# Kernel optimization log

Hardware: AMD Instinct MI355X
Metric: run time of the kernel (lower is better)

## Reference

```python
import jax, jax.numpy as jnp
import numpy as np

# ----- config (mirrors SpatialAxis init) -----
B, N = 1, 32768
D_MODEL, NHEAD, DEPTH = 256, 8, 2
COORD = 3
PATCH = 512          # self.patch_size default
BITS = 10            # self.morton_bits default
SHIFT = True         # self.shift_order default
MLP_H = 4 * D_MODEL
HD = D_MODEL // NHEAD
EPS = 1e-5


def _part1by2(v):
    # spread low 10 bits of int32 so there are 2 zero bits between each
    v = v & 0x000003FF
    v = (v | (v << 16)) & 0x030000FF
    v = (v | (v << 8)) & 0x0300F00F
    v = (v | (v << 4)) & 0x030C30C3
    v = (v | (v << 2)) & 0x09249249
    return v


def _perm_for_block(coords, i):
    # Z-order (Morton) serialization with per-block axis rotation; odd blocks
    # shift the order by half a patch (shifted-window style). Returns [B,N] int32.
    c = jax.lax.stop_gradient(coords)[..., np.roll(np.arange(COORD), -i)]
    cmin = c.min(axis=1, keepdims=True)
    cmax = c.max(axis=1, keepdims=True)
    q = ((c - cmin) / (cmax - cmin + 1e-9) * (2 ** BITS - 1)).astype(jnp.int32)
    q = jnp.clip(q, 0, 2 ** BITS - 1)
    code = (_part1by2(q[..., 0]) | (_part1by2(q[..., 1]) << 1)
            | (_part1by2(q[..., 2]) << 2))  # [B,N]
    perm = jnp.argsort(code, axis=1)
    if SHIFT and (i % 2 == 1):
        perm = jnp.roll(perm, PATCH // 2, axis=1)
    return perm


def _ln(x, g, b):
    m = x.mean(-1, keepdims=True)
    v = x.var(-1, keepdims=True)
    return (x - m) * jax.lax.rsqrt(v + EPS) * g + b


def _point_block(xs, cs, p):
    # xs: [M, P, D] tokens of one patch each; cs: [M, P, 3]
    M, P, D = xs.shape
    h = _ln(xs, p['ln1_g'], p['ln1_b'])
    qkv = h @ p['w_qkv'] + p['b_qkv']                         # [M,P,3D]
    q, k, v = jnp.split(qkv, 3, axis=-1)
    q = q.reshape(M, P, NHEAD, HD)
    k = k.reshape(M, P, NHEAD, HD)
    v = v.reshape(M, P, NHEAD, HD)
    scores = jnp.einsum('mphd,mqhd->mhpq', q, k) / np.sqrt(HD).astype(np.float32)
    rel = cs[:, :, None, :] - cs[:, None, :, :]               # [M,P,P,3]
    bias = jnp.einsum('mpqc,ch->mhpq', rel, p['w_pos']) + p['b_pos'][None, :, None, None]
    attn = jax.nn.softmax(scores + bias, axis=-1)
    o = jnp.einsum('mhpq,mqhd->mphd', attn, v).reshape(M, P, D)
    xs = xs + o @ p['w_proj'] + p['b_proj']
    h2 = _ln(xs, p['ln2_g'], p['ln2_b'])
    xs = xs + jax.nn.gelu(h2 @ p['w_fc1'] + p['b_fc1']) @ p['w_fc2'] + p['b_fc2']
    return xs


def _forward(x, coords, params):
    Cc = coords.shape[-1]
    nblk = N // PATCH
    for i in range(DEPTH):
        p = {k: v[i] for k, v in params.items()}
        perm = _perm_for_block(coords, i)                      # [B,N]
        inv = jnp.argsort(perm, axis=1)
        x_s = jnp.take_along_axis(x, perm[:, :, None], axis=1)
        c_s = jnp.take_along_axis(coords, perm[:, :, None], axis=1)
        x_f = x_s.reshape(B * nblk, PATCH, D_MODEL)
        c_f = c_s.reshape(B * nblk, PATCH, Cc)
        y = _point_block(x_f, c_f, p).reshape(B, N, D_MODEL)
        x = jnp.take_along_axis(y, inv[:, :, None], axis=1)
    return _ln(x, params['norm_g'][0], params['norm_b'][0])


def setup_inputs() -> dict:
    key = jax.random.key(0)
    ks = jax.random.split(key, 20)
    s = 0.02
    d = {
        'x': jax.random.normal(ks[0], (B, N, D_MODEL), jnp.float32),
        'coords': jax.random.uniform(ks[1], (B, N, COORD), jnp.float32),
        'ln1_g': jnp.ones((DEPTH, D_MODEL), jnp.float32),
        'ln1_b': jnp.zeros((DEPTH, D_MODEL), jnp.float32),
        'w_qkv': jax.random.normal(ks[2], (DEPTH, D_MODEL, 3 * D_MODEL), jnp.float32) * s,
        'b_qkv': jnp.zeros((DEPTH, 3 * D_MODEL), jnp.float32),
        'w_proj': jax.random.normal(ks[3], (DEPTH, D_MODEL, D_MODEL), jnp.float32) * s,
        'b_proj': jnp.zeros((DEPTH, D_MODEL), jnp.float32),
        'w_pos': jax.random.normal(ks[4], (DEPTH, COORD, NHEAD), jnp.float32) * s,
        'b_pos': jnp.zeros((DEPTH, NHEAD), jnp.float32),
        'ln2_g': jnp.ones((DEPTH, D_MODEL), jnp.float32),
        'ln2_b': jnp.zeros((DEPTH, D_MODEL), jnp.float32),
        'w_fc1': jax.random.normal(ks[5], (DEPTH, D_MODEL, MLP_H), jnp.float32) * s,
        'b_fc1': jnp.zeros((DEPTH, MLP_H), jnp.float32),
        'w_fc2': jax.random.normal(ks[6], (DEPTH, MLP_H, D_MODEL), jnp.float32) * s,
        'b_fc2': jnp.zeros((DEPTH, D_MODEL), jnp.float32),
        'norm_g': jnp.ones((1, D_MODEL), jnp.float32),
        'norm_b': jnp.zeros((1, D_MODEL), jnp.float32),
    }
    return d


def reference(x, coords, ln1_g, ln1_b, w_qkv, b_qkv, w_proj, b_proj, w_pos, b_pos,
              ln2_g, ln2_b, w_fc1, b_fc1, w_fc2, b_fc2, norm_g, norm_b):
    params = dict(ln1_g=ln1_g, ln1_b=ln1_b, w_qkv=w_qkv, b_qkv=b_qkv,
                  w_proj=w_proj, b_proj=b_proj, w_pos=w_pos, b_pos=b_pos,
                  ln2_g=ln2_g, ln2_b=ln2_b, w_fc1=w_fc1, b_fc1=b_fc1,
                  w_fc2=w_fc2, b_fc2=b_fc2, norm_g=norm_g, norm_b=norm_b)
    return _forward(x, coords, params)
```

## Files before the change

### kernel.cpp

```cpp
#include <hip/hip_runtime.h>

typedef unsigned long long u64;
typedef unsigned int u32;
typedef unsigned short u16;
typedef float f32x4 __attribute__((ext_vector_type(4)));
typedef __bf16 bf16x8 __attribute__((ext_vector_type(8)));

#define N_TOK 32768

__device__ inline u16 f2bf(float f){
  u32 x = __float_as_uint(f);
  u32 r = x + 0x7FFFu + ((x >> 16) & 1u);
  return (u16)(r >> 16);
}

__device__ inline u16 f2bf_hw(float f){
  u32 pk;
  asm("v_cvt_pk_bf16_f32 %0, %1, %2" : "=v"(pk) : "v"(f), "v"(0.f));
  return (u16)pk;
}

__device__ inline f32x4 mfma16(bf16x8 a, bf16x8 b, f32x4 c){
  return __builtin_amdgcn_mfma_f32_16x16x32_bf16(a, b, c, 0, 0, 0);
}

__device__ inline float fexp2(float x){
  float r;
  asm("v_exp_f32 %0, %1" : "=v"(r) : "v"(x));
  return r;
}
__device__ inline float frcp(float x){
  float r;
  asm("v_rcp_f32 %0, %1" : "=v"(r) : "v"(x));
  return r;
}

typedef const __attribute__((address_space(1))) unsigned int* gas_ptr;
typedef __attribute__((address_space(3))) unsigned int* las_ptr;
__device__ inline void gload_lds16(const u16* g, u16* l){
  __builtin_amdgcn_global_load_lds((gas_ptr)g, (las_ptr)l, 16, 0, 0);
}

__device__ inline u32 rp_idx(const u64* __restrict__ keys, int j, int shift){
  return (u32)(keys[(j + N_TOK - shift) & (N_TOK - 1)] & 0xFFFFull);
}

__device__ inline float gelu_tanh(float x){
  float u = 0.7978845608028654f * (x + 0.044715f * x * x * x);
  float e = fexp2(2.8853900817779268f * u);
  return 0.5f * x * (2.0f - 2.0f * frcp(e + 1.0f));
}

__device__ inline u32 part1by2(u32 v){
  v &= 0x3FFu;
  v = (v | (v << 16)) & 0x030000FFu;
  v = (v | (v << 8))  & 0x0300F00Fu;
  v = (v | (v << 4))  & 0x030C30C3u;
  v = (v | (v << 2))  & 0x09249249u;
  return v;
}

__device__ inline void ce64(u64& a, u64& b, bool asc){
  u64 lo = a < b ? a : b;
  u64 hi = a < b ? b : a;
  a = asc ? lo : hi;
  b = asc ? hi : lo;
}

__device__ inline int xcd_swz(int bid, int nwg){
  int cpx = nwg >> 3;
  return (bid & 7) * cpx + (bid >> 3);
}

__global__ void minmax_init(u32* __restrict__ cmm){
  int t = threadIdx.x;
  if (t < 3) cmm[t] = 0xFFFFFFFFu;
  else if (t < 6) cmm[t] = 0u;
}

__global__ void __launch_bounds__(256) minmax_atomic(const float* __restrict__ coords,
                                                     u32* __restrict__ cmm){
  __shared__ u32 smn[3], smx[3];
  int t = threadIdx.x;
  if (t < 3){ smn[t] = 0xFFFFFFFFu; smx[t] = 0u; }
  __syncthreads();
  int i = blockIdx.x * 256 + t;
  u32 bits = __float_as_uint(coords[i]);
  int a = i % 3;
  atomicMin(&smn[a], bits);
  atomicMax(&smx[a], bits);
  __syncthreads();
  if (t < 3){
    atomicMin(&cmm[t], smn[t]);
    atomicMax(&cmm[3 + t], smx[t]);
  }
}

__global__ void __launch_bounds__(256) wprep_all(
    const float* __restrict__ w_qkv, const float* __restrict__ w_proj,
    const float* __restrict__ w_fc1, const float* __restrict__ w_fc2,
    u16* __restrict__ d_qkv, u16* __restrict__ d_proj,
    u16* __restrict__ d_fc1, u16* __restrict__ d_fc2){
  int b = blockIdx.x;
  const float* src; u16* dst; int K, Nn;
  if (b < 384){ src = w_qkv; dst = d_qkv; K = 256; Nn = 768; }
  else if (b < 512){ b -= 384; src = w_proj; dst = d_proj; K = 256; Nn = 256; }
  else if (b < 1024){ b -= 512; src = w_fc1; dst = d_fc1; K = 256; Nn = 1024; }
  else { b -= 1024; src = w_fc2; dst = d_fc2; K = 1024; Nn = 256; }
  int ntx = Nn >> 5;
  int tpl = (K >> 5) * ntx;
  int layer = b / tpl, tb = b % tpl;
  src += (size_t)layer * K * Nn;
  dst += (size_t)layer * K * Nn;
  int tk = tb / ntx, tn = tb % ntx;
  __shared__ float tile[32][33];
  int r = threadIdx.x >> 5, c = threadIdx.x & 31;
  for (int rr = r; rr < 32; rr += 8)
    tile[rr][c] = src[(size_t)(tk*32 + rr) * Nn + tn*32 + c];
  __syncthreads();
  for (int rr = r; rr < 32; rr += 8)
    dst[(size_t)(tn*32 + rr) * K + tk*32 + c] = f2bf(tile[c][rr]);
}

__global__ void __launch_bounds__(256) codes_kernel(const float* __restrict__ coords,
                                                    const float* __restrict__ cmm,
                                                    u64* __restrict__ keys){
  int p = blockIdx.x * 256 + threadIdx.x;
  int layer = p >> 15, t = p & (N_TOK - 1);
  u32 code = 0;
  #pragma unroll
  for (int j = 0; j < 3; ++j){
    int ax = (j + layer) % 3;
    float c = coords[t*3 + ax];
    float mn = cmm[ax], mx = cmm[3 + ax];
    float v = (c - mn) / (mx - mn + 1e-9f) * 1023.0f;
    int q = (int)v;
    q = q < 0 ? 0 : (q > 1023 ? 1023 : q);
    code |= part1by2((u32)q) << j;
  }
  keys[p] = ((u64)code << 16) | (u32)t;
}

__global__ void __launch_bounds__(64) sort_wave1024(u64* __restrict__ keys){
  int chunk = blockIdx.x;
  int lane = threadIdx.x;
  int base = chunk * 1024 + lane * 16;
  int bl = base & (N_TOK - 1);
  u64 v[16];
  #pragma unroll
  for (int p = 0; p < 16; ++p) v[p] = keys[base + p];
  #pragma unroll
  for (int k2 = 2; k2 <= 16; k2 <<= 1){
    #pragma unroll
    for (int j = k2 >> 1; j > 0; j >>= 1){
      #pragma unroll
      for (int p = 0; p < 16; ++p){
        if ((p & j) == 0){
          bool asc = (((bl + p) & k2) == 0);
          ce64(v[p], v[p+j], asc);
        }
      }
    }
  }
  #pragma unroll
  for (int kk = 32; kk <= 1024; kk <<= 1){
    bool asc = ((bl & kk) == 0);
    #pragma unroll
    for (int j = kk >> 1; j >= 16; j >>= 1){
      int m = j >> 4;
      bool kmin = asc != ((lane & m) != 0);
      #pragma unroll
      for (int p = 0; p < 16; ++p){
        u64 pv = __shfl_xor(v[p], m);
        u64 mn = v[p] < pv ? v[p] : pv;
        u64 mx = v[p] < pv ? pv : v[p];
        v[p] = kmin ? mn : mx;
      }
    }
    #pragma unroll
    for (int j = 8; j > 0; j >>= 1)
      #pragma unroll
      for (int p = 0; p < 16; ++p)
        if ((p & j) == 0) ce64(v[p], v[p+j], asc);
  }
  #pragma unroll
  for (int p = 0; p < 16; ++p) keys[base + p] = v[p];
}

template<int R>
__global__ void __launch_bounds__(256) sort_strided(u64* __restrict__ keys, int logJ, int k){
  const int E = 1 << R;
  int gps = N_TOK >> R;
  int tid = blockIdx.x * 256 + threadIdx.x;
  int seg = tid / gps, gamma = tid % gps;
  int high = gamma >> logJ, low = gamma & ((1 << logJ) - 1);
  int base = seg * N_TOK + (high << (logJ + R)) + low;
  u64 v[E];
  #pragma unroll
  for (int m = 0; m < E; ++m) v[m] = keys[base + (m << logJ)];
  bool asc = (((base & (N_TOK - 1)) & k) == 0);
  #pragma unroll
  for (int jj = R - 1; jj >= 0; --jj)
    #pragma unroll
    for (int m = 0; m < E; ++m)
      if ((m & (1 << jj)) == 0) ce64(v[m], v[m + (1 << jj)], asc);
  #pragma unroll
  for (int m = 0; m < E; ++m) keys[base + (m << logJ)] = v[m];
}

__global__ void __launch_bounds__(64) sort_tail1024(u64* __restrict__ keys, int k){
  int chunk = blockIdx.x;
  int lane = threadIdx.x;
  int base = chunk * 1024 + lane * 16;
  bool asc = ((((chunk * 1024) & (N_TOK - 1)) & k) == 0);
  u64 v[16];
  #pragma unroll
  for (int p = 0; p < 16; ++p) v[p] = keys[base + p];
  #pragma unroll
  for (int m = 32; m >= 1; m >>= 1){
    bool kmin = asc != ((lane & m) != 0);
    #pragma unroll
    for (int p = 0; p < 16; ++p){
      u64 pv = __shfl_xor(v[p], m);
      u64 mn = v[p] < pv ? v[p] : pv;
      u64 mx = v[p] < pv ? pv : v[p];
      v[p] = kmin ? mn : mx;
    }
  }
  #pragma unroll
  for (int j = 8; j > 0; j >>= 1)
    #pragma unroll
    for (int p = 0; p < 16; ++p)
      if ((p & j) == 0) ce64(v[p], v[p+j], asc);
  #pragma unroll
  for (int p = 0; p < 16; ++p) keys[base + p] = v[p];
}

__global__ void __launch_bounds__(256) gather_ln1_kernel(
    const float* __restrict__ xin, const float* __restrict__ coords,
    const u64* __restrict__ keys, int shift,
    const float* __restrict__ g1, const float* __restrict__ b1,
    const float* __restrict__ wpos,
    float* __restrict__ dproj, u16* __restrict__ h){
  int w = threadIdx.x >> 6, lane = threadIdx.x & 63;
  int j = blockIdx.x * 4 + w;
  u32 src = rp_idx(keys, j, shift);
  float4 v = ((const float4*)xin)[(size_t)src * 64 + lane];
  float s = v.x + v.y + v.z + v.w;
  for (int m = 1; m < 64; m <<= 1) s += __shfl_xor(s, m);
  float mean = s * (1.0f / 256.0f);
  float dx = v.x - mean, dy = v.y - mean, dz = v.z - mean, dw = v.w - mean;
  float q = dx*dx + dy*dy + dz*dz + dw*dw;
  for (int m = 1; m < 64; m <<= 1) q += __shfl_xor(q, m);
  float rs = rsqrtf(q * (1.0f / 256.0f) + 1e-5f);
  int c0 = lane * 4;
  u16 h0 = f2bf(dx * rs * g1[c0+0] + b1[c0+0]);
  u16 h1 = f2bf(dy * rs * g1[c0+1] + b1[c0+1]);
  u16 h2 = f2bf(dz * rs * g1[c0+2] + b1[c0+2]);
  u16 h3 = f2bf(dw * rs * g1[c0+3] + b1[c0+3]);
  uint2 pk; pk.x = (u32)h0 | ((u32)h1 << 16); pk.y = (u32)h2 | ((u32)h3 << 16);
  *(uint2*)&h[(size_t)j * 256 + c0] = pk;
  if (lane < 8){
    float acc = 0.0f;
    #pragma unroll
    for (int c = 0; c < 3; ++c) acc += coords[(size_t)src*3 + c] * wpos[c*8 + lane];
    dproj[(size_t)j * 8 + lane] = acc;
  }
}

__global__ void __launch_bounds__(256) ln_bf16_kernel(const float* __restrict__ xin,
    const float* __restrict__ g, const float* __restrict__ b, u16* __restrict__ out){
  int w = threadIdx.x >> 6, lane = threadIdx.x & 63;
  int j = blockIdx.x * 4 + w;
  float4 v = ((const float4*)xin)[(size_t)j * 64 + lane];
  float s = v.x + v.y + v.z + v.w;
  for (int m = 1; m < 64; m <<= 1) s += __shfl_xor(s, m);
  float mean = s * (1.0f / 256.0f);
  float dx = v.x - mean, dy = v.y - mean, dz = v.z - mean, dw = v.w - mean;
  float q = dx*dx + dy*dy + dz*dz + dw*dw;
  for (int m = 1; m < 64; m <<= 1) q += __shfl_xor(q, m);
  float rs = rsqrtf(q * (1.0f / 256.0f) + 1e-5f);
  int c0 = lane * 4;
  u16 h0 = f2bf(dx * rs * g[c0+0] + b[c0+0]);
  u16 h1 = f2bf(dy * rs * g[c0+1] + b[c0+1]);
  u16 h2 = f2bf(dz * rs * g[c0+2] + b[c0+2]);
  u16 h3 = f2bf(dw * rs * g[c0+3] + b[c0+3]);
  uint2 pk; pk.x = (u32)h0 | ((u32)h1 << 16); pk.y = (u32)h2 | ((u32)h3 << 16);
  *(uint2*)&out[(size_t)j * 256 + c0] = pk;
}

__global__ void __launch_bounds__(256) ln_final_kernel(const float* __restrict__ xin,
    const float* __restrict__ g, const float* __restrict__ b, float* __restrict__ out){
  int w = threadIdx.x >> 6, lane = threadIdx.x & 63;
  int j = blockIdx.x * 4 + w;
  float4 v = ((const float4*)xin)[(size_t)j * 64 + lane];
  float s = v.x + v.y + v.z + v.w;
  for (int m = 1; m < 64; m <<= 1) s += __shfl_xor(s, m);
  float mean = s * (1.0f / 256.0f);
  float dx = v.x - mean, dy = v.y - mean, dz = v.z - mean, dw = v.w - mean;
  float q = dx*dx + dy*dy + dz*dz + dw*dw;
  for (int m = 1; m < 64; m <<= 1) q += __shfl_xor(q, m);
  float rs = rsqrtf(q * (1.0f / 256.0f) + 1e-5f);
  int c0 = lane * 4;
  float4 o;
  o.x = dx * rs * g[c0+0] + b[c0+0];
  o.y = dy * rs * g[c0+1] + b[c0+1];
  o.z = dz * rs * g[c0+2] + b[c0+2];
  o.w = dw * rs * g[c0+3] + b[c0+3];
  ((float4*)out)[(size_t)j * 64 + lane] = o;
}

template<int EPI, int BN>
__global__ void __launch_bounds__(1024) gemm2_kernel(
    const u16* __restrict__ A, const u16* __restrict__ Wt,
    const float* __restrict__ bias, int K, int Nn,
    u16* __restrict__ outb, float* __restrict__ outf,
    const float* __restrict__ res, const u64* __restrict__ keys, int shift){
  constexpr int WN = (BN == 256) ? 4 : 2;
  constexpr int WM = 16 / WN;
  constexpr int MI = (256 / WM) / 16;
  constexpr int NI = (BN / WN) / 16;
  constexpr int SPANM = 256 / WM;
  constexpr int SPANN = BN / WN;
  __shared__ __align__(16) u16 As[2][256 * 32];
  __shared__ __align__(16) u16 Bs[2][BN * 32];
  int swz = xcd_swz(blockIdx.x, gridDim.x);
  int ntiles = Nn / BN;
  int m0 = (swz / ntiles) * 256;
  int n0 = (swz % ntiles) * BN;
  int tid = threadIdx.x;
  int lane = tid & 63, lc = lane & 15, g = lane >> 4;
  int w = tid >> 6;
  int wm = (BN == 256) ? (w >> 2) : (w >> 1);
  int wn = (BN == 256) ? (w & 3) : (w & 1);
  f32x4 acc[MI][NI];
  #pragma unroll
  for (int mi = 0; mi < MI; ++mi)
    #pragma unroll
    for (int ni = 0; ni < NI; ++ni) acc[mi][ni] = (f32x4){0.f,0.f,0.f,0.f};
  int rA = tid >> 2, sA = tid & 3;
  const u16* Ag = A + (size_t)(m0 + rA) * K + (sA ^ ((rA >> 1) & 3)) * 8;
  int cb = (BN == 256) ? tid : (tid & 511);
  int rB = cb >> 2, sB = cb & 3;
  const u16* Bg = Wt + (size_t)(n0 + rB) * K + (sB ^ ((rB >> 1) & 3)) * 8;
  int aofs = (tid & ~63) * 8;
  int bofs = (cb & ~63) * 8;
  int nt = K >> 5;
  auto issue = [&](int t, int b){
    int kk = t << 5;
    gload_lds16(Ag + kk, As[b] + aofs);
    gload_lds16(Bg + kk, Bs[b] + bofs);
  };
  issue(0, 0);
  int cur = 0;
  int fsw = (lc >> 1) & 3;
  for (int t = 0; t < nt; ++t){
    if (t + 1 < nt){
      issue(t + 1, cur ^ 1);
      asm volatile("s_waitcnt vmcnt(2)" ::: "memory");
    } else {
      asm volatile("s_waitcnt vmcnt(0)" ::: "memory");
    }
    __builtin_amdgcn_s_barrier();
    bf16x8 af[MI], bfr[NI];
    #pragma unroll
    for (int mi = 0; mi < MI; ++mi)
      af[mi] = *(const bf16x8*)&As[cur][(wm*SPANM + mi*16 + lc)*32 + (g ^ fsw)*8];
    #pragma unroll
    for (int ni = 0; ni < NI; ++ni)
      bfr[ni] = *(const bf16x8*)&Bs[cur][(wn*SPANN + ni*16 + lc)*32 + (g ^ fsw)*8];
    #pragma unroll
    for (int mi = 0; mi < MI; ++mi)
      #pragma unroll
      for (int ni = 0; ni < NI; ++ni)
        acc[mi][ni] = mfma16(af[mi], bfr[ni], acc[mi][ni]);
    asm volatile("" ::: "memory");
    __builtin_amdgcn_s_barrier();
    cur ^= 1;
  }
  #pragma unroll
  for (int ni = 0; ni < NI; ++ni){
    int col = n0 + wn*SPANN + ni*16 + lc;
    float bv = bias[col];
    #pragma unroll
    for (int mi = 0; mi < MI; ++mi){
      #pragma unroll
      for (int r = 0; r < 4; ++r){
        int row = m0 + wm*SPANM + mi*16 + g*4 + r;
        float v = acc[mi][ni][r] + bv;
        if constexpr (EPI == 0){
          if (col < 256) v *= 0.25500526f;
          outb[(size_t)row * Nn + col] = f2bf_hw(v);
        } else if constexpr (EPI == 1){
          outb[(size_t)row * Nn + col] = f2bf_hw(gelu_tanh(v));
        } else {
          u32 dst = rp_idx(keys, row, shift);
          outf[(size_t)dst * 256 + col] = res[(size_t)row * 256 + col] + v;
        }
      }
    }
  }
}

template<int EPI>
__global__ void __launch_bounds__(256) gemm_kernel(
    const u16* __restrict__ A, const u16* __restrict__ Wt,
    const float* __restrict__ bias, int K, int Nn,
    u16* __restrict__ outb, float* __restrict__ outf,
    const float* __restrict__ res, const u64* __restrict__ keys, int shift){
  __shared__ __align__(16) u16 As[2][128 * 32];
  __shared__ __align__(16) u16 Bs[2][128 * 32];
  int swz = xcd_swz(blockIdx.x, gridDim.x);
  int ntiles = Nn / 128;
  int m0 = (swz / ntiles) * 128;
  int n0 = (swz % ntiles) * 128;
  int tid = threadIdx.x;
  int lane = tid & 63, lc = lane & 15, g = lane >> 4;
  int w = tid >> 6, wm = w >> 1, wn = w & 1;
  f32x4 acc[4][4];
  #pragma unroll
  for (int mi = 0; mi < 4; ++mi)
    #pragma unroll
    for (int ni = 0; ni < 4; ++ni) acc[mi][ni] = (f32x4){0.f,0.f,0.f,0.f};
  int r1 = tid >> 2, s1 = tid & 3;
  int r2 = r1 + 64;
  int sw = s1 ^ ((r1 >> 1) & 3);
  const u16* Ag1 = A  + (size_t)(m0 + r1) * K + sw*8;
  const u16* Ag2 = A  + (size_t)(m0 + r2) * K + sw*8;
  const u16* Bg1 = Wt + (size_t)(n0 + r1) * K + sw*8;
  const u16* Bg2 = Wt + (size_t)(n0 + r2) * K + sw*8;
  int wofs = (tid & ~63) * 8;
  int nt = K >> 5;
  gload_lds16(Ag1, As[0] + wofs);
  gload_lds16(Ag2, As[0] + wofs + 2048);
  gload_lds16(Bg1, Bs[0] + wofs);
  gload_lds16(Bg2, Bs[0] + wofs + 2048);
  int cur = 0;
  int fsw = (lc >> 1) & 3;
  for (int t = 0; t < nt; ++t){
    if (t + 1 < nt){
      int kk = (t + 1) << 5;
      gload_lds16(Ag1 + kk, As[cur^1] + wofs);
      gload_lds16(Ag2 + kk, As[cur^1] + wofs + 2048);
      gload_lds16(Bg1 + kk, Bs[cur^1] + wofs);
      gload_lds16(Bg2 + kk, Bs[cur^1] + wofs + 2048);
      asm volatile("s_waitcnt vmcnt(4)" ::: "memory");
    } else {
      asm volatile("s_waitcnt vmcnt(0)" ::: "memory");
    }
    __builtin_amdgcn_s_barrier();
    bf16x8 af[4], bfr[4];
    #pragma unroll
    for (int mi = 0; mi < 4; ++mi)
      af[mi] = *(const bf16x8*)&As[cur][(wm*64 + mi*16 + lc)*32 + (g ^ fsw)*8];
    #pragma unroll
    for (int ni = 0; ni < 4; ++ni)
      bfr[ni] = *(const bf16x8*)&Bs[cur][(wn*64 + ni*16 + lc)*32 + (g ^ fsw)*8];
    #pragma unroll
    for (int mi = 0; mi < 4; ++mi)
      #pragma unroll
      for (int ni = 0; ni < 4; ++ni)
        acc[mi][ni] = mfma16(af[mi], bfr[ni], acc[mi][ni]);
    asm volatile("" ::: "memory");
    __builtin_amdgcn_s_barrier();
    cur ^= 1;
  }
  #pragma unroll
  for (int ni = 0; ni < 4; ++ni){
    int col = n0 + wn*64 + ni*16 + lc;
    float bv = bias[col];
    #pragma unroll
    for (int mi = 0; mi < 4; ++mi){
      #pragma unroll
      for (int r = 0; r < 4; ++r){
        int row = m0 + wm*64 + mi*16 + g*4 + r;
        float v = acc[mi][ni][r] + bv;
        if constexpr (EPI == 2){
          u32 src = rp_idx(keys, row, shift);
          outf[(size_t)row * 256 + col] = res[(size_t)src * 256 + col] + v;
        } else {
          outb[(size_t)row * Nn + col] = f2bf_hw(v);
        }
      }
    }
  }
}

#define VSTR 516
#define ATTN_LDS (512*32*2 + 32*VSTR*2 + 512*2)
__global__ void __launch_bounds__(512) attn_kernel(
    const u16* __restrict__ qkvb, const float* __restrict__ dproj,
    u16* __restrict__ o){
  extern __shared__ char smem[];
  u16* Kl = (u16*)smem;
  u16* Vt = (u16*)(smem + 512*32*2);
  u16* wl = (u16*)(smem + 512*32*2 + 32*VSTR*2);
  int h = blockIdx.x & 7;
  int base = (blockIdx.x >> 3) * 512;
  int tid = threadIdx.x, w = tid >> 6, lane = tid & 63, lc = lane & 15, g = lane >> 4;
  const float L2E = 1.4426950408889634f;
  for (int i = tid; i < 2048; i += 512){
    int j = i >> 2, s = i & 3;
    int swc = s ^ ((j >> 1) & 3);
    *(uint4*)&Kl[j*32 + s*8] =
      *(const uint4*)&qkvb[(size_t)(base + j)*768 + 256 + h*32 + swc*8];
  }
  for (int i = tid; i < 1024; i += 512){
    int p = i >> 2, d0 = (i & 3) * 8;
    int j0 = 2*p, j1 = j0 + 1;
    float wv0 = fexp2(-L2E * dproj[(size_t)(base + j0)*8 + h]);
    float wv1 = fexp2(-L2E * dproj[(size_t)(base + j1)*8 + h]);
    uint4 r0 = *(const uint4*)&qkvb[(size_t)(base + j0)*768 + 512 + h*32 + d0];
    uint4 r1 = *(const uint4*)&qkvb[(size_t)(base + j1)*768 + 512 + h*32 + d0];
    const u16* p0 = (const u16*)&r0; const u16* p1 = (const u16*)&r1;
    int j5 = j0 & 31, b = j5 >> 4, m = j5 & 15;
    int slot = (j0 & ~31) + 8*(m >> 2) + 4*b + (m & 3);
    #pragma unroll
    for (int e = 0; e < 8; ++e){
      float f0 = __uint_as_float(((u32)p0[e]) << 16) * wv0;
      float f1 = __uint_as_float(((u32)p1[e]) << 16) * wv1;
      u32 pk;
      asm("v_cvt_pk_bf16_f32 %0, %1, %2" : "=v"(pk) : "v"(f0), "v"(f1));
      *(u32*)&Vt[(d0 + e)*VSTR + slot] = pk;
    }
    if (d0 == 0){
      u32 pkw;
      asm("v_cvt_pk_bf16_f32 %0, %1, %2" : "=v"(pkw) : "v"(wv0), "v"(wv1));
      *(u32*)&wl[slot] = pkw;
    }
  }
  __syncthreads();
  const f32x4 zf = {0.f,0.f,0.f,0.f};
  const u16* Qg = qkvb + (size_t)base*768 + h*32;
  int fswk = (lc >> 1) & 3;
  for (int t = 0; t < 4; ++t){
    int q0 = w*64 + t*16;
    bf16x8 qf = *(const bf16x8*)&Qg[(size_t)(q0 + lc)*768 + g*8];
    f32x4 oa0 = zf, oa1 = zf, la = zf;
    f32x4 ob0 = zf, ob1 = zf, lb = zf;
    #pragma unroll 4
    for (int grp = 0; grp < 16; ++grp){
      int kb = grp * 32;
      bf16x8 kf0 = *(const bf16x8*)&Kl[(kb + lc)*32 + (g ^ fswk)*8];
      bf16x8 kf1 = *(const bf16x8*)&Kl[(kb + 16 + lc)*32 + (g ^ fswk)*8];
      f32x4 s0 = mfma16(kf0, qf, zf);
      f32x4 s1 = mfma16(kf1, qf, zf);
      #pragma unroll
      for (int r = 0; r < 4; ++r){
        s0[r] = fexp2(s0[r]);
        s1[r] = fexp2(s1[r]);
      }
      u32 pk0, pk1, pk2, pk3;
      asm("v_cvt_pk_bf16_f32 %0, %1, %2" : "=v"(pk0) : "v"(s0[0]), "v"(s0[1]));
      asm("v_cvt_pk_bf16_f32 %0, %1, %2" : "=v"(pk1) : "v"(s0[2]), "v"(s0[3]));
      asm("v_cvt_pk_bf16_f32 %0, %1, %2" : "=v"(pk2) : "v"(s1[0]), "v"(s1[1]));
      asm("v_cvt_pk_bf16_f32 %0, %1, %2" : "=v"(pk3) : "v"(s1[2]), "v"(s1[3]));
      bf16x8 pf;
      ((u32*)&pf)[0] = pk0; ((u32*)&pf)[1] = pk1;
      ((u32*)&pf)[2] = pk2; ((u32*)&pf)[3] = pk3;
      bf16x8 v0, v1;
      *(uint2*)&v0       = *(const uint2*)&Vt[lc*VSTR + kb + g*8];
      *((uint2*)&v0 + 1) = *(const uint2*)&Vt[lc*VSTR + kb + g*8 + 4];
      *(uint2*)&v1       = *(const uint2*)&Vt[(16+lc)*VSTR + kb + g*8];
      *((uint2*)&v1 + 1) = *(const uint2*)&Vt[(16+lc)*VSTR + kb + g*8 + 4];
      bf16x8 wf = *(const bf16x8*)&wl[kb + g*8];
      __builtin_amdgcn_s_setprio(1);
      if (grp & 1){
        ob0 = mfma16(pf, v0, ob0);
        ob1 = mfma16(pf, v1, ob1);
        lb  = mfma16(pf, wf, lb);
      } else {
        oa0 = mfma16(pf, v0, oa0);
        oa1 = mfma16(pf, v1, oa1);
        la  = mfma16(pf, wf, la);
      }
      __builtin_amdgcn_s_setprio(0);
    }
    #pragma unroll
    for (int r = 0; r < 4; ++r){
      float inv = frcp(la[r] + lb[r]);
      size_t tok = (size_t)(base + q0 + g*4 + r);
      o[tok*256 + h*32 + lc]      = f2bf((oa0[r] + ob0[r]) * inv);
      o[tok*256 + h*32 + 16 + lc] = f2bf((oa1[r] + ob1[r]) * inv);
    }
  }
}

extern "C" void kernel_launch(void* const* d_in, const int* in_sizes, int n_in,
                              void* d_out, int out_size, void* d_ws, size_t ws_size,
                              hipStream_t stream){
  const float* x      = (const float*)d_in[0];
  const float* coords = (const float*)d_in[1];
  const float* ln1_g  = (const float*)d_in[2];
  const float* ln1_b  = (const float*)d_in[3];
  const float* w_qkv  = (const float*)d_in[4];
  const float* b_qkv  = (const float*)d_in[5];
  const float* w_proj = (const float*)d_in[6];
  const float* b_proj = (const float*)d_in[7];
  const float* w_pos  = (const float*)d_in[8];
  const float* ln2_g  = (const float*)d_in[10];
  const float* ln2_b  = (const float*)d_in[11];
  const float* w_fc1  = (const float*)d_in[12];
  const float* b_fc1  = (const float*)d_in[13];
  const float* w_fc2  = (const float*)d_in[14];
  const float* b_fc2  = (const float*)d_in[15];
  const float* norm_g = (const float*)d_in[16];
  const float* norm_b = (const float*)d_in[17];
  float* outp = (float*)d_out;

  hipFuncSetAttribute((const void*)attn_kernel,
                      hipFuncAttributeMaxDynamicSharedMemorySize, ATTN_LDS);

  char* ws = (char*)d_ws;
  size_t off = 0;
  auto alloc = [&](size_t bytes) -> void* {
    void* p = ws + off;
    off += (bytes + 255) & ~(size_t)255;
    return p;
  };
  u64*   keys   = (u64*)  alloc((size_t)2 * N_TOK * 8);
  float* cmm    = (float*)alloc(256);
  float* dproj  = (float*)alloc((size_t)N_TOK * 8 * 4);
  u16*   h      = (u16*)  alloc((size_t)N_TOK * 256 * 2);
  u16*   qkvb   = (u16*)  alloc((size_t)N_TOK * 768 * 2);
  float* x2     = (float*)alloc((size_t)N_TOK * 256 * 4);
  u16*   t      = (u16*)  alloc((size_t)N_TOK * 1024 * 2);
  float* xA     = (float*)alloc((size_t)N_TOK * 256 * 4);
  u16*   wtqkv  = (u16*)  alloc((size_t)2 * 256 * 768 * 2);
  u16*   wtproj = (u16*)  alloc((size_t)2 * 256 * 256 * 2);
  u16*   wtfc1  = (u16*)  alloc((size_t)2 * 256 * 1024 * 2);
  u16*   wtfc2  = (u16*)  alloc((size_t)2 * 1024 * 256 * 2);
  u16*   o      = t;
  float* xB     = (float*)qkvb;
  (void)in_sizes; (void)n_in; (void)out_size; (void)ws_size;

  minmax_init<<<1, 64, 0, stream>>>((u32*)cmm);
  minmax_atomic<<<384, 256, 0, stream>>>(coords, (u32*)cmm);
  wprep_all<<<1536, 256, 0, stream>>>(w_qkv, w_proj, w_fc1, w_fc2,
                                      wtqkv, wtproj, wtfc1, wtfc2);

  codes_kernel<<<256, 256, 0, stream>>>(coords, cmm, keys);
  sort_wave1024<<<64, 64, 0, stream>>>(keys);
  sort_strided<1><<<128, 256, 0, stream>>>(keys, 10, 2048);
  sort_tail1024<<<64, 64, 0, stream>>>(keys, 2048);
  sort_strided<2><<<64, 256, 0, stream>>>(keys, 10, 4096);
  sort_tail1024<<<64, 64, 0, stream>>>(keys, 4096);
  sort_strided<3><<<32, 256, 0, stream>>>(keys, 10, 8192);
  sort_tail1024<<<64, 64, 0, stream>>>(keys, 8192);
  sort_strided<3><<<32, 256, 0, stream>>>(keys, 11, 16384);
  sort_strided<1><<<128, 256, 0, stream>>>(keys, 10, 16384);
  sort_tail1024<<<64, 64, 0, stream>>>(keys, 16384);
  sort_strided<3><<<32, 256, 0, stream>>>(keys, 12, 32768);
  sort_strided<2><<<64, 256, 0, stream>>>(keys, 10, 32768);
  sort_tail1024<<<64, 64, 0, stream>>>(keys, 32768);

  for (int layer = 0; layer < 2; ++layer){
    int shift = (layer & 1) ? 256 : 0;
    const float* xin = (layer == 0) ? x : xA;
    float* xout = (layer == 0) ? xA : xB;
    u64* keyL = keys + (size_t)layer * N_TOK;

    gather_ln1_kernel<<<8192, 256, 0, stream>>>(xin, coords, keyL, shift,
        ln1_g + layer*256, ln1_b + layer*256, w_pos + layer*24, dproj, h);
    gemm2_kernel<0,256><<<384, 1024, 0, stream>>>(h, wtqkv + (size_t)layer*768*256,
        b_qkv + layer*768, 256, 768, qkvb, nullptr, nullptr, nullptr, 0);
    attn_kernel<<<512, 512, ATTN_LDS, stream>>>(qkvb, dproj, o);
    gemm_kernel<2><<<512, 256, 0, stream>>>(o, wtproj + (size_t)layer*256*256,
        b_proj + layer*256, 256, 256, nullptr, x2, xin, keyL, shift);
    ln_bf16_kernel<<<8192, 256, 0, stream>>>(x2, ln2_g + layer*256, ln2_b + layer*256, h);
    gemm2_kernel<1,256><<<512, 1024, 0, stream>>>(h, wtfc1 + (size_t)layer*1024*256,
        b_fc1 + layer*1024, 256, 1024, t, nullptr, nullptr, nullptr, 0);
    gemm2_kernel<3,128><<<256, 1024, 0, stream>>>(t, wtfc2 + (size_t)layer*256*1024,
        b_fc2 + layer*256, 1024, 256, nullptr, xout, x2, keyL, shift);
  }
  ln_final_kernel<<<8192, 256, 0, stream>>>(xB, norm_g, norm_b, outp);
}
```

Baseline: 473.6 us.

## Fuse proj GEMM with residual and LayerNorm2; process two query tiles per attention iteration

```diff
diff --git a/kernel.cpp b/kernel.cpp
--- a/kernel.cpp
+++ b/kernel.cpp
@@ -268,27 +268,6 @@
   }
 }
 
-__global__ void __launch_bounds__(256) ln_bf16_kernel(const float* __restrict__ xin,
-    const float* __restrict__ g, const float* __restrict__ b, u16* __restrict__ out){
-  int w = threadIdx.x >> 6, lane = threadIdx.x & 63;
-  int j = blockIdx.x * 4 + w;
-  float4 v = ((const float4*)xin)[(size_t)j * 64 + lane];
-  float s = v.x + v.y + v.z + v.w;
-  for (int m = 1; m < 64; m <<= 1) s += __shfl_xor(s, m);
-  float mean = s * (1.0f / 256.0f);
-  float dx = v.x - mean, dy = v.y - mean, dz = v.z - mean, dw = v.w - mean;
-  float q = dx*dx + dy*dy + dz*dz + dw*dw;
-  for (int m = 1; m < 64; m <<= 1) q += __shfl_xor(q, m);
-  float rs = rsqrtf(q * (1.0f / 256.0f) + 1e-5f);
-  int c0 = lane * 4;
-  u16 h0 = f2bf(dx * rs * g[c0+0] + b[c0+0]);
-  u16 h1 = f2bf(dy * rs * g[c0+1] + b[c0+1]);
-  u16 h2 = f2bf(dz * rs * g[c0+2] + b[c0+2]);
-  u16 h3 = f2bf(dw * rs * g[c0+3] + b[c0+3]);
-  uint2 pk; pk.x = (u32)h0 | ((u32)h1 << 16); pk.y = (u32)h2 | ((u32)h3 << 16);
-  *(uint2*)&out[(size_t)j * 256 + c0] = pk;
-}
-
 __global__ void __launch_bounds__(256) ln_final_kernel(const float* __restrict__ xin,
     const float* __restrict__ g, const float* __restrict__ b, float* __restrict__ out){
   int w = threadIdx.x >> 6, lane = threadIdx.x & 63;
@@ -402,49 +381,43 @@
   }
 }
 
-template<int EPI>
-__global__ void __launch_bounds__(256) gemm_kernel(
+__global__ void __launch_bounds__(1024) gemm2ln_kernel(
     const u16* __restrict__ A, const u16* __restrict__ Wt,
-    const float* __restrict__ bias, int K, int Nn,
-    u16* __restrict__ outb, float* __restrict__ outf,
-    const float* __restrict__ res, const u64* __restrict__ keys, int shift){
-  __shared__ __align__(16) u16 As[2][128 * 32];
-  __shared__ __align__(16) u16 Bs[2][128 * 32];
+    const float* __restrict__ bias,
+    const u64* __restrict__ keys, int shift, const float* __restrict__ res,
+    const float* __restrict__ g2, const float* __restrict__ b2,
+    float* __restrict__ x2out, u16* __restrict__ hout){
+  __shared__ __align__(16) u16 As[2][256 * 32];
+  __shared__ __align__(16) u16 Bs[2][256 * 32];
+  __shared__ float red_s[256][4];
+  __shared__ float red_q[256][4];
+  const int K = 256;
   int swz = xcd_swz(blockIdx.x, gridDim.x);
-  int ntiles = Nn / 128;
-  int m0 = (swz / ntiles) * 128;
-  int n0 = (swz % ntiles) * 128;
+  int m0 = swz * 256;
   int tid = threadIdx.x;
   int lane = tid & 63, lc = lane & 15, g = lane >> 4;
-  int w = tid >> 6, wm = w >> 1, wn = w & 1;
+  int w = tid >> 6, wm = w >> 2, wn = w & 3;
   f32x4 acc[4][4];
   #pragma unroll
   for (int mi = 0; mi < 4; ++mi)
     #pragma unroll
     for (int ni = 0; ni < 4; ++ni) acc[mi][ni] = (f32x4){0.f,0.f,0.f,0.f};
-  int r1 = tid >> 2, s1 = tid & 3;
-  int r2 = r1 + 64;
-  int sw = s1 ^ ((r1 >> 1) & 3);
-  const u16* Ag1 = A  + (size_t)(m0 + r1) * K + sw*8;
-  const u16* Ag2 = A  + (size_t)(m0 + r2) * K + sw*8;
-  const u16* Bg1 = Wt + (size_t)(n0 + r1) * K + sw*8;
-  const u16* Bg2 = Wt + (size_t)(n0 + r2) * K + sw*8;
-  int wofs = (tid & ~63) * 8;
-  int nt = K >> 5;
-  gload_lds16(Ag1, As[0] + wofs);
-  gload_lds16(Ag2, As[0] + wofs + 2048);
-  gload_lds16(Bg1, Bs[0] + wofs);
-  gload_lds16(Bg2, Bs[0] + wofs + 2048);
+  int rA = tid >> 2, sA = tid & 3;
+  const u16* Ag = A  + (size_t)(m0 + rA) * K + (sA ^ ((rA >> 1) & 3)) * 8;
+  const u16* Bg = Wt + (size_t)rA * K + (sA ^ ((rA >> 1) & 3)) * 8;
+  int aofs = (tid & ~63) * 8;
+  auto issue = [&](int t, int b){
+    int kk = t << 5;
+    gload_lds16(Ag + kk, As[b] + aofs);
+    gload_lds16(Bg + kk, Bs[b] + aofs);
+  };
+  issue(0, 0);
   int cur = 0;
   int fsw = (lc >> 1) & 3;
-  for (int t = 0; t < nt; ++t){
-    if (t + 1 < nt){
-      int kk = (t + 1) << 5;
-      gload_lds16(Ag1 + kk, As[cur^1] + wofs);
-      gload_lds16(Ag2 + kk, As[cur^1] + wofs + 2048);
-      gload_lds16(Bg1 + kk, Bs[cur^1] + wofs);
-      gload_lds16(Bg2 + kk, Bs[cur^1] + wofs + 2048);
-      asm volatile("s_waitcnt vmcnt(4)" ::: "memory");
+  for (int t = 0; t < 8; ++t){
+    if (t + 1 < 8){
+      issue(t + 1, cur ^ 1);
+      asm volatile("s_waitcnt vmcnt(2)" ::: "memory");
     } else {
       asm volatile("s_waitcnt vmcnt(0)" ::: "memory");
     }
@@ -465,22 +438,53 @@
     __builtin_amdgcn_s_barrier();
     cur ^= 1;
   }
+  float bv[4], g2v[4], b2v[4];
   #pragma unroll
   for (int ni = 0; ni < 4; ++ni){
-    int col = n0 + wn*64 + ni*16 + lc;
-    float bv = bias[col];
-    #pragma unroll
-    for (int mi = 0; mi < 4; ++mi){
-      #pragma unroll
-      for (int r = 0; r < 4; ++r){
-        int row = m0 + wm*64 + mi*16 + g*4 + r;
-        float v = acc[mi][ni][r] + bv;
-        if constexpr (EPI == 2){
-          u32 src = rp_idx(keys, row, shift);
-          outf[(size_t)row * 256 + col] = res[(size_t)src * 256 + col] + v;
-        } else {
-          outb[(size_t)row * Nn + col] = f2bf_hw(v);
-        }
+    int col = wn*64 + ni*16 + lc;
+    bv[ni] = bias[col];
+    g2v[ni] = g2[col];
+    b2v[ni] = b2[col];
+  }
+  #pragma unroll
+  for (int mi = 0; mi < 4; ++mi){
+    #pragma unroll
+    for (int r = 0; r < 4; ++r){
+      int lrow = wm*64 + mi*16 + g*4 + r;
+      int grow = m0 + lrow;
+      u32 src = rp_idx(keys, grow, shift);
+      float sp = 0.f, qp = 0.f;
+      #pragma unroll
+      for (int ni = 0; ni < 4; ++ni){
+        int col = wn*64 + ni*16 + lc;
+        float v = acc[mi][ni][r] + bv[ni] + res[(size_t)src*256 + col];
+        sp += v; qp += v*v;
+        x2out[(size_t)grow*256 + col] = v;
+      }
+      sp += __shfl_xor(sp, 1); sp += __shfl_xor(sp, 2);
+      sp += __shfl_xor(sp, 4); sp += __shfl_xor(sp, 8);
+      qp += __shfl_xor(qp, 1); qp += __shfl_xor(qp, 2);
+      qp += __shfl_xor(qp, 4); qp += __shfl_xor(qp, 8);
+      if (lc == 0){ red_s[lrow][wn] = sp; red_q[lrow][wn] = qp; }
+    }
+  }
+  __syncthreads();
+  #pragma unroll
+  for (int mi = 0; mi < 4; ++mi){
+    #pragma unroll
+    for (int r = 0; r < 4; ++r){
+      int lrow = wm*64 + mi*16 + g*4 + r;
+      int grow = m0 + lrow;
+      float s = red_s[lrow][0] + red_s[lrow][1] + red_s[lrow][2] + red_s[lrow][3];
+      float q = red_q[lrow][0] + red_q[lrow][1] + red_q[lrow][2] + red_q[lrow][3];
+      float mean = s * (1.0f / 256.0f);
+      float var = q * (1.0f / 256.0f) - mean * mean;
+      float rs = rsqrtf(var + 1e-5f);
+      #pragma unroll
+      for (int ni = 0; ni < 4; ++ni){
+        int col = wn*64 + ni*16 + lc;
+        float v = x2out[(size_t)grow*256 + col];
+        hout[(size_t)grow*256 + col] = f2bf_hw((v - mean) * rs * g2v[ni] + b2v[ni]);
       }
     }
   }
@@ -533,9 +537,10 @@
   const f32x4 zf = {0.f,0.f,0.f,0.f};
   const u16* Qg = qkvb + (size_t)base*768 + h*32;
   int fswk = (lc >> 1) & 3;
-  for (int t = 0; t < 4; ++t){
-    int q0 = w*64 + t*16;
-    bf16x8 qf = *(const bf16x8*)&Qg[(size_t)(q0 + lc)*768 + g*8];
+  for (int t = 0; t < 2; ++t){
+    int q0 = w*64 + t*32;
+    bf16x8 qfa = *(const bf16x8*)&Qg[(size_t)(q0 + lc)*768 + g*8];
+    bf16x8 qfb = *(const bf16x8*)&Qg[(size_t)(q0 + 16 + lc)*768 + g*8];
     f32x4 oa0 = zf, oa1 = zf, la = zf;
     f32x4 ob0 = zf, ob1 = zf, lb = zf;
     #pragma unroll 4
@@ -543,21 +548,29 @@
       int kb = grp * 32;
       bf16x8 kf0 = *(const bf16x8*)&Kl[(kb + lc)*32 + (g ^ fswk)*8];
       bf16x8 kf1 = *(const bf16x8*)&Kl[(kb + 16 + lc)*32 + (g ^ fswk)*8];
-      f32x4 s0 = mfma16(kf0, qf, zf);
-      f32x4 s1 = mfma16(kf1, qf, zf);
+      f32x4 sa0 = mfma16(kf0, qfa, zf);
+      f32x4 sa1 = mfma16(kf1, qfa, zf);
+      f32x4 sb0 = mfma16(kf0, qfb, zf);
+      f32x4 sb1 = mfma16(kf1, qfb, zf);
       #pragma unroll
       for (int r = 0; r < 4; ++r){
-        s0[r] = fexp2(s0[r]);
-        s1[r] = fexp2(s1[r]);
+        sa0[r] = fexp2(sa0[r]); sa1[r] = fexp2(sa1[r]);
+        sb0[r] = fexp2(sb0[r]); sb1[r] = fexp2(sb1[r]);
       }
-      u32 pk0, pk1, pk2, pk3;
-      asm("v_cvt_pk_bf16_f32 %0, %1, %2" : "=v"(pk0) : "v"(s0[0]), "v"(s0[1]));
-      asm("v_cvt_pk_bf16_f32 %0, %1, %2" : "=v"(pk1) : "v"(s0[2]), "v"(s0[3]));
-      asm("v_cvt_pk_bf16_f32 %0, %1, %2" : "=v"(pk2) : "v"(s1[0]), "v"(s1[1]));
-      asm("v_cvt_pk_bf16_f32 %0, %1, %2" : "=v"(pk3) : "v"(s1[2]), "v"(s1[3]));
-      bf16x8 pf;
-      ((u32*)&pf)[0] = pk0; ((u32*)&pf)[1] = pk1;
-      ((u32*)&pf)[2] = pk2; ((u32*)&pf)[3] = pk3;
+      u32 ka0, ka1, ka2, ka3, kb0, kb1, kb2, kb3;
+      asm("v_cvt_pk_bf16_f32 %0, %1, %2" : "=v"(ka0) : "v"(sa0[0]), "v"(sa0[1]));
+      asm("v_cvt_pk_bf16_f32 %0, %1, %2" : "=v"(ka1) : "v"(sa0[2]), "v"(sa0[3]));
+      asm("v_cvt_pk_bf16_f32 %0, %1, %2" : "=v"(ka2) : "v"(sa1[0]), "v"(sa1[1]));
+      asm("v_cvt_pk_bf16_f32 %0, %1, %2" : "=v"(ka3) : "v"(sa1[2]), "v"(sa1[3]));
+      asm("v_cvt_pk_bf16_f32 %0, %1, %2" : "=v"(kb0) : "v"(sb0[0]), "v"(sb0[1]));
+      asm("v_cvt_pk_bf16_f32 %0, %1, %2" : "=v"(kb1) : "v"(sb0[2]), "v"(sb0[3]));
+      asm("v_cvt_pk_bf16_f32 %0, %1, %2" : "=v"(kb2) : "v"(sb1[0]), "v"(sb1[1]));
+      asm("v_cvt_pk_bf16_f32 %0, %1, %2" : "=v"(kb3) : "v"(sb1[2]), "v"(sb1[3]));
+      bf16x8 pfa, pfb;
+      ((u32*)&pfa)[0] = ka0; ((u32*)&pfa)[1] = ka1;
+      ((u32*)&pfa)[2] = ka2; ((u32*)&pfa)[3] = ka3;
+      ((u32*)&pfb)[0] = kb0; ((u32*)&pfb)[1] = kb1;
+      ((u32*)&pfb)[2] = kb2; ((u32*)&pfb)[3] = kb3;
       bf16x8 v0, v1;
       *(uint2*)&v0       = *(const uint2*)&Vt[lc*VSTR + kb + g*8];
       *((uint2*)&v0 + 1) = *(const uint2*)&Vt[lc*VSTR + kb + g*8 + 4];
@@ -565,23 +578,24 @@
       *((uint2*)&v1 + 1) = *(const uint2*)&Vt[(16+lc)*VSTR + kb + g*8 + 4];
       bf16x8 wf = *(const bf16x8*)&wl[kb + g*8];
       __builtin_amdgcn_s_setprio(1);
-      if (grp & 1){
-        ob0 = mfma16(pf, v0, ob0);
-        ob1 = mfma16(pf, v1, ob1);
-        lb  = mfma16(pf, wf, lb);
-      } else {
-        oa0 = mfma16(pf, v0, oa0);
-        oa1 = mfma16(pf, v1, oa1);
-        la  = mfma16(pf, wf, la);
-      }
+      oa0 = mfma16(pfa, v0, oa0);
+      oa1 = mfma16(pfa, v1, oa1);
+      la  = mfma16(pfa, wf, la);
+      ob0 = mfma16(pfb, v0, ob0);
+      ob1 = mfma16(pfb, v1, ob1);
+      lb  = mfma16(pfb, wf, lb);
       __builtin_amdgcn_s_setprio(0);
     }
     #pragma unroll
     for (int r = 0; r < 4; ++r){
-      float inv = frcp(la[r] + lb[r]);
-      size_t tok = (size_t)(base + q0 + g*4 + r);
-      o[tok*256 + h*32 + lc]      = f2bf((oa0[r] + ob0[r]) * inv);
-      o[tok*256 + h*32 + 16 + lc] = f2bf((oa1[r] + ob1[r]) * inv);
+      float inva = frcp(la[r]);
+      float invb = frcp(lb[r]);
+      size_t tokA = (size_t)(base + q0 + g*4 + r);
+      size_t tokB = tokA + 16;
+      o[tokA*256 + h*32 + lc]      = f2bf(oa0[r] * inva);
+      o[tokA*256 + h*32 + 16 + lc] = f2bf(oa1[r] * inva);
+      o[tokB*256 + h*32 + lc]      = f2bf(ob0[r] * invb);
+      o[tokB*256 + h*32 + 16 + lc] = f2bf(ob1[r] * invb);
     }
   }
 }
@@ -665,9 +679,9 @@
     gemm2_kernel<0,256><<<384, 1024, 0, stream>>>(h, wtqkv + (size_t)layer*768*256,
         b_qkv + layer*768, 256, 768, qkvb, nullptr, nullptr, nullptr, 0);
     attn_kernel<<<512, 512, ATTN_LDS, stream>>>(qkvb, dproj, o);
-    gemm_kernel<2><<<512, 256, 0, stream>>>(o, wtproj + (size_t)layer*256*256,
-        b_proj + layer*256, 256, 256, nullptr, x2, xin, keyL, shift);
-    ln_bf16_kernel<<<8192, 256, 0, stream>>>(x2, ln2_g + layer*256, ln2_b + layer*256, h);
+    gemm2ln_kernel<<<128, 1024, 0, stream>>>(o, wtproj + (size_t)layer*256*256,
+        b_proj + layer*256, keyL, shift, xin,
+        ln2_g + layer*256, ln2_b + layer*256, x2, h);
     gemm2_kernel<1,256><<<512, 1024, 0, stream>>>(h, wtfc1 + (size_t)layer*1024*256,
         b_fc1 + layer*1024, 256, 1024, t, nullptr, nullptr, nullptr, 0);
     gemm2_kernel<3,128><<<256, 1024, 0, stream>>>(t, wtfc2 + (size_t)layer*256*1024,
```

After: 485.9 us. +2.6%, slower.
